# Kernel optimization log

Hardware: AMD Instinct MI355X
Metric: run time of the kernel (lower is better)

The kernel has to match this reference:

```python
import jax, jax.numpy as jnp
import numpy as np

DIMS = 256
HID = 512


def setup_inputs() -> dict:
    key = jax.random.key(0)
    ks = jax.random.split(key, 12)
    s = 0.1
    inp = {
        'x': jax.random.normal(ks[0], (64, 2048, DIMS), dtype=jnp.float32),
        'h': jnp.zeros((64, HID), jnp.float32),
        'c': jnp.zeros((64, HID), jnp.float32),
        'W_j': jax.random.normal(ks[1], (DIMS, HID), jnp.float32) * s,
        'W_i': jax.random.normal(ks[2], (DIMS, HID), jnp.float32) * s,
        'W_f': jax.random.normal(ks[3], (DIMS, HID), jnp.float32) * s,
        'W_o': jax.random.normal(ks[4], (DIMS, HID), jnp.float32) * s,
        'U_j': jax.random.normal(ks[5], (HID, HID), jnp.float32) * s,
        'U_i': jax.random.normal(ks[6], (HID, HID), jnp.float32) * s,
        'U_f': jax.random.normal(ks[7], (HID, HID), jnp.float32) * s,
        'U_o': jax.random.normal(ks[8], (HID, HID), jnp.float32) * s,
        'b_j': jnp.zeros((1, HID), jnp.float32),
        'b_i': jnp.zeros((1, HID), jnp.float32),
        'b_f': jnp.zeros((1, HID), jnp.float32),
        'b_o': jnp.zeros((1, HID), jnp.float32),
        'W_y': jax.random.normal(ks[9], (HID, DIMS), jnp.float32) * s,
        'b_y': jnp.zeros((1, DIMS), jnp.float32),
    }
    return inp


def reference(x, h, c, W_j, W_i, W_f, W_o, U_j, U_i, U_f, U_o,
              b_j, b_i, b_f, b_o, W_y, b_y):
    # Precompute input projections for all timesteps: [B,T,H] -> [T,B,H]
    xj = jnp.einsum('btd,dh->tbh', x, W_j) + b_j
    xi = jnp.einsum('btd,dh->tbh', x, W_i) + b_i
    xf = jnp.einsum('btd,dh->tbh', x, W_f) + b_f
    xo = jnp.einsum('btd,dh->tbh', x, W_o) + b_o

    def step(carry, xs):
        h, c = carry
        pj, pi, pf, po = xs
        # NOTE: module defaults -> j,i,o sigmoid; f tanh; cell activation tanh
        j = jax.nn.sigmoid(pj + h @ U_j)
        i = jax.nn.sigmoid(pi + h @ U_i)
        f = jnp.tanh(pf + h @ U_f)
        o = jax.nn.sigmoid(po + h @ U_o)
        c = f * c + i * j
        h = o * jnp.tanh(c)
        return (h, c), h

    (h_last, c_last), hs = jax.lax.scan(step, (h, c), (xj, xi, xf, xo))
    # hs: [T,B,H] -> y_hat: [B,T,dims]
    y_hat = jnp.einsum('tbh,hd->btd', hs, W_y) + b_y
    return y_hat, h_last, c_last
```

## Files before the change

kernel.cpp:

```cpp
#include <hip/hip_runtime.h>


typedef __attribute__((ext_vector_type(8))) short bf16x8;
typedef __attribute__((ext_vector_type(4))) float f32x4;

#define T_STEPS 2048
#define DIMS 256
#define HID 512

#define NPACK_U  1048576
#define NPACK_WX 524288
#define NPACK_WY 131072

#define OFF_UHI   0u
#define OFF_ULO   2097152u
#define OFF_WXHI  4194304u
#define OFF_WXLO  5242880u
#define OFF_WYHI  6291456u
#define OFF_WYLO  6553600u
#define OFF_HBUF  6815744u
#define OFF_FLAGS 7077888u

__device__ __forceinline__ unsigned short f2bf(float f) {
    unsigned u = __float_as_uint(f);
    return (unsigned short)((u + 0x7fffu + ((u >> 16) & 1u)) >> 16);
}
__device__ __forceinline__ float bf2f(unsigned short h) {
    return __uint_as_float((unsigned)h << 16);
}
__device__ __forceinline__ void split2(float f, unsigned short& hi, unsigned short& lo) {
    hi = f2bf(f);
    lo = f2bf(f - bf2f(hi));
}
__device__ __forceinline__ float sigf(float x) { return 1.0f / (1.0f + __expf(-x)); }
__device__ __forceinline__ float tanhfast(float x) { return 2.0f * sigf(2.0f * x) - 1.0f; }

__global__ void lstm_prep(const float* __restrict__ Uj, const float* __restrict__ Ui,
                          const float* __restrict__ Uf, const float* __restrict__ Uo,
                          const float* __restrict__ Wj, const float* __restrict__ Wi,
                          const float* __restrict__ Wf, const float* __restrict__ Wo,
                          const float* __restrict__ Wy,
                          unsigned short* __restrict__ Uph, unsigned short* __restrict__ Upl,
                          unsigned short* __restrict__ Wxh, unsigned short* __restrict__ Wxl,
                          unsigned short* __restrict__ Wyh, unsigned short* __restrict__ Wyl,
                          unsigned* __restrict__ flags) {
    int idx = blockIdx.x * 256 + threadIdx.x;
    if (idx < NPACK_U) {
        int j = idx & 7, l = (idx >> 3) & 63, ks = (idx >> 9) & 15, nt = (idx >> 13) & 7, s = (idx >> 16) & 15;
        int gate = nt >> 1;
        int hu = s * 32 + (nt & 1) * 16 + (l & 15);
        int k = ks * 32 + ((l >> 4) << 3) + j;
        const float* U = (gate == 0) ? Uj : (gate == 1) ? Ui : (gate == 2) ? Uf : Uo;
        unsigned short hi, lo; split2(U[k * HID + hu], hi, lo);
        Uph[idx] = hi; Upl[idx] = lo;
    } else if (idx < NPACK_U + NPACK_WX) {
        int i2 = idx - NPACK_U;
        int j = i2 & 7, l = (i2 >> 3) & 63, ks = (i2 >> 9) & 7, nt = (i2 >> 12) & 7, s = (i2 >> 15) & 15;
        int gate = nt >> 1;
        int hu = s * 32 + (nt & 1) * 16 + (l & 15);
        int k = ks * 32 + ((l >> 4) << 3) + j;
        const float* W = (gate == 0) ? Wj : (gate == 1) ? Wi : (gate == 2) ? Wf : Wo;
        unsigned short hi, lo; split2(W[k * HID + hu], hi, lo);
        Wxh[i2] = hi; Wxl[i2] = lo;
    } else if (idx < NPACK_U + NPACK_WX + NPACK_WY) {
        int i3 = idx - NPACK_U - NPACK_WX;
        int j = i3 & 7, l = (i3 >> 3) & 63, ks = (i3 >> 9) & 15, s = (i3 >> 13) & 15;
        int k = ks * 32 + ((l >> 4) << 3) + j;
        int col = s * 16 + (l & 15);
        unsigned short hi, lo; split2(Wy[k * DIMS + col], hi, lo);
        Wyh[i3] = hi; Wyl[i3] = lo;
    } else if (idx < NPACK_U + NPACK_WX + NPACK_WY + 64) {
        flags[idx - (NPACK_U + NPACK_WX + NPACK_WY)] = 0u;
    }
}

__global__ __launch_bounds__(256, 1) void lstm_scan(
    const float* __restrict__ x, const float* __restrict__ h0, const float* __restrict__ c0,
    const float* __restrict__ bj_g, const float* __restrict__ bi_g,
    const float* __restrict__ bf_g, const float* __restrict__ bo_g,
    const float* __restrict__ by_g,
    const unsigned short* __restrict__ Uph, const unsigned short* __restrict__ Upl,
    const unsigned short* __restrict__ Wxph, const unsigned short* __restrict__ Wxpl,
    const unsigned short* __restrict__ Wyph, const unsigned short* __restrict__ Wypl,
    unsigned* __restrict__ hbuf32, unsigned* __restrict__ flags,
    float* __restrict__ out)
{
    __shared__ unsigned short xsh[16][264];
    __shared__ unsigned short xsl[16][264];
    __shared__ unsigned short hsh[16][520];
    __shared__ unsigned short hsl[16][520];
    __shared__ float pre[8][16][17];
    __shared__ float yp[4][16][17];
    __shared__ float cbuf[16][32];

    const int tid = threadIdx.x;
    const int wv = tid >> 6;
    const int l = tid & 63;
    const int quad = l >> 4;
    const int lm = l & 15;
    const int g = blockIdx.x >> 4;
    const int s = blockIdx.x & 15;

    bf16x8 bUh[2][16], bUl[2][16], bWxh[2][8], bWxl[2][8], bWyh[4], bWyl[4];
    {
        const bf16x8* UH = reinterpret_cast<const bf16x8*>(Uph);
        const bf16x8* UL = reinterpret_cast<const bf16x8*>(Upl);
        const bf16x8* WH = reinterpret_cast<const bf16x8*>(Wxph);
        const bf16x8* WL = reinterpret_cast<const bf16x8*>(Wxpl);
        const bf16x8* YH = reinterpret_cast<const bf16x8*>(Wyph);
        const bf16x8* YL = reinterpret_cast<const bf16x8*>(Wypl);
        #pragma unroll
        for (int i = 0; i < 2; ++i) {
            int nt = 2 * wv + i;
            #pragma unroll
            for (int ks = 0; ks < 16; ++ks) {
                bUh[i][ks] = UH[((s * 8 + nt) * 16 + ks) * 64 + l];
                bUl[i][ks] = UL[((s * 8 + nt) * 16 + ks) * 64 + l];
            }
            #pragma unroll
            for (int ks = 0; ks < 8; ++ks) {
                bWxh[i][ks] = WH[((s * 8 + nt) * 8 + ks) * 64 + l];
                bWxl[i][ks] = WL[((s * 8 + nt) * 8 + ks) * 64 + l];
            }
        }
        #pragma unroll
        for (int q = 0; q < 4; ++q) {
            bWyh[q] = YH[(s * 16 + wv * 4 + q) * 64 + l];
            bWyl[q] = YL[(s * 16 + wv * 4 + q) * 64 + l];
        }
    }

    const int rr = tid >> 4;
    const int uu = (tid & 15) * 2;
    cbuf[rr][uu]     = c0[(size_t)(g * 16 + rr) * HID + s * 32 + uu];
    cbuf[rr][uu + 1] = c0[(size_t)(g * 16 + rr) * HID + s * 32 + uu + 1];
    float bj0 = bj_g[s * 32 + uu], bj1 = bj_g[s * 32 + uu + 1];
    float bi0 = bi_g[s * 32 + uu], bi1 = bi_g[s * 32 + uu + 1];
    float bf0 = bf_g[s * 32 + uu], bf1 = bf_g[s * 32 + uu + 1];
    float bo0 = bo_g[s * 32 + uu], bo1 = bo_g[s * 32 + uu + 1];
    const float by = by_g[s * 16 + (tid & 15)];

    const int rS = tid >> 4;
    const int cS16 = (tid & 15) * 16;
    const int cS32 = (tid & 15) * 32;
    long long budget = 1ll << 24;

    __syncthreads();

    for (int t = 0; t < T_STEPS; ++t) {
        {
            const float4* xv = reinterpret_cast<const float4*>(
                x + (size_t)(g * 16 + rS) * (T_STEPS * DIMS) + (size_t)t * DIMS + cS16);
            uint4* xdh = reinterpret_cast<uint4*>(&xsh[rS][cS16]);
            uint4* xdl = reinterpret_cast<uint4*>(&xsl[rS][cS16]);
            #pragma unroll
            for (int k = 0; k < 2; ++k) {
                float4 fa = xv[2 * k], fb = xv[2 * k + 1];
                unsigned short h0_, l0_, h1_, l1_, h2_, l2_, h3_, l3_;
                unsigned short h4_, l4_, h5_, l5_, h6_, l6_, h7_, l7_;
                split2(fa.x, h0_, l0_); split2(fa.y, h1_, l1_);
                split2(fa.z, h2_, l2_); split2(fa.w, h3_, l3_);
                split2(fb.x, h4_, l4_); split2(fb.y, h5_, l5_);
                split2(fb.z, h6_, l6_); split2(fb.w, h7_, l7_);
                uint4 uh, ul;
                uh.x = (unsigned)h0_ | ((unsigned)h1_ << 16);
                uh.y = (unsigned)h2_ | ((unsigned)h3_ << 16);
                uh.z = (unsigned)h4_ | ((unsigned)h5_ << 16);
                uh.w = (unsigned)h6_ | ((unsigned)h7_ << 16);
                ul.x = (unsigned)l0_ | ((unsigned)l1_ << 16);
                ul.y = (unsigned)l2_ | ((unsigned)l3_ << 16);
                ul.z = (unsigned)l4_ | ((unsigned)l5_ << 16);
                ul.w = (unsigned)l6_ | ((unsigned)l7_ << 16);
                xdh[k] = uh; xdl[k] = ul;
            }
        }
        __syncthreads();
        f32x4 acc0 = {0.f, 0.f, 0.f, 0.f}, acc1 = {0.f, 0.f, 0.f, 0.f};
        #pragma unroll
        for (int ks = 0; ks < 8; ++ks) {
            bf16x8 ah = *reinterpret_cast<const bf16x8*>(&xsh[lm][ks * 32 + quad * 8]);
            bf16x8 al = *reinterpret_cast<const bf16x8*>(&xsl[lm][ks * 32 + quad * 8]);
            acc0 = __builtin_amdgcn_mfma_f32_16x16x32_bf16(ah, bWxh[0][ks], acc0, 0, 0, 0);
            acc0 = __builtin_amdgcn_mfma_f32_16x16x32_bf16(al, bWxh[0][ks], acc0, 0, 0, 0);
            acc0 = __builtin_amdgcn_mfma_f32_16x16x32_bf16(ah, bWxl[0][ks], acc0, 0, 0, 0);
            acc1 = __builtin_amdgcn_mfma_f32_16x16x32_bf16(ah, bWxh[1][ks], acc1, 0, 0, 0);
            acc1 = __builtin_amdgcn_mfma_f32_16x16x32_bf16(al, bWxh[1][ks], acc1, 0, 0, 0);
            acc1 = __builtin_amdgcn_mfma_f32_16x16x32_bf16(ah, bWxl[1][ks], acc1, 0, 0, 0);
        }

        if (t > 0) {
            const unsigned target = (unsigned)t;
            while (budget > 0) {
                unsigned v = (l < 16)
                    ? __hip_atomic_load(&flags[g * 16 + l], __ATOMIC_RELAXED, __HIP_MEMORY_SCOPE_AGENT)
                    : target;
                if (__all((int)(v >= target))) break;
                --budget;
            }
            asm volatile("" ::: "memory");
            const unsigned base = (unsigned)(((t - 1) & 1) * 32768) + (unsigned)(g * 16 + rS) * 256
                                  + (unsigned)(tid & 15) * 16;
            const unsigned long long* sh = reinterpret_cast<const unsigned long long*>(hbuf32 + base);
            const unsigned long long* sl = reinterpret_cast<const unsigned long long*>(hbuf32 + 16384 + base);
            unsigned long long vh[8], vl[8];
            #pragma unroll
            for (int k = 0; k < 8; ++k)
                vh[k] = __hip_atomic_load(&sh[k], __ATOMIC_RELAXED, __HIP_MEMORY_SCOPE_AGENT);
            #pragma unroll
            for (int k = 0; k < 8; ++k)
                vl[k] = __hip_atomic_load(&sl[k], __ATOMIC_RELAXED, __HIP_MEMORY_SCOPE_AGENT);
            unsigned long long* dh = reinterpret_cast<unsigned long long*>(&hsh[rS][cS32]);
            unsigned long long* dl = reinterpret_cast<unsigned long long*>(&hsl[rS][cS32]);
            #pragma unroll
            for (int k = 0; k < 8; ++k) dh[k] = vh[k];
            #pragma unroll
            for (int k = 0; k < 8; ++k) dl[k] = vl[k];
        } else {
            const float4* hv = reinterpret_cast<const float4*>(
                h0 + (size_t)(g * 16 + rS) * HID + cS32);
            unsigned* hdh = reinterpret_cast<unsigned*>(&hsh[rS][cS32]);
            unsigned* hdl = reinterpret_cast<unsigned*>(&hsl[rS][cS32]);
            #pragma unroll
            for (int k = 0; k < 8; ++k) {
                float4 f = hv[k];
                unsigned short a0, b0, a1, b1, a2, b2, a3, b3;
                split2(f.x, a0, b0); split2(f.y, a1, b1);
                split2(f.z, a2, b2); split2(f.w, a3, b3);
                hdh[2 * k]     = (unsigned)a0 | ((unsigned)a1 << 16);
                hdh[2 * k + 1] = (unsigned)a2 | ((unsigned)a3 << 16);
                hdl[2 * k]     = (unsigned)b0 | ((unsigned)b1 << 16);
                hdl[2 * k + 1] = (unsigned)b2 | ((unsigned)b3 << 16);
            }
        }
        __syncthreads();

        #pragma unroll
        for (int ks = 0; ks < 16; ++ks) {
            bf16x8 ah = *reinterpret_cast<const bf16x8*>(&hsh[lm][ks * 32 + quad * 8]);
            bf16x8 al = *reinterpret_cast<const bf16x8*>(&hsl[lm][ks * 32 + quad * 8]);
            acc0 = __builtin_amdgcn_mfma_f32_16x16x32_bf16(ah, bUh[0][ks], acc0, 0, 0, 0);
            acc0 = __builtin_amdgcn_mfma_f32_16x16x32_bf16(al, bUh[0][ks], acc0, 0, 0, 0);
            acc0 = __builtin_amdgcn_mfma_f32_16x16x32_bf16(ah, bUl[0][ks], acc0, 0, 0, 0);
            acc1 = __builtin_amdgcn_mfma_f32_16x16x32_bf16(ah, bUh[1][ks], acc1, 0, 0, 0);
            acc1 = __builtin_amdgcn_mfma_f32_16x16x32_bf16(al, bUh[1][ks], acc1, 0, 0, 0);
            acc1 = __builtin_amdgcn_mfma_f32_16x16x32_bf16(ah, bUl[1][ks], acc1, 0, 0, 0);
        }
        f32x4 yacc = {0.f, 0.f, 0.f, 0.f};
        if (t > 0) {
            #pragma unroll
            for (int q = 0; q < 4; ++q) {
                bf16x8 ah = *reinterpret_cast<const bf16x8*>(&hsh[lm][(wv * 4 + q) * 32 + quad * 8]);
                bf16x8 al = *reinterpret_cast<const bf16x8*>(&hsl[lm][(wv * 4 + q) * 32 + quad * 8]);
                yacc = __builtin_amdgcn_mfma_f32_16x16x32_bf16(ah, bWyh[q], yacc, 0, 0, 0);
                yacc = __builtin_amdgcn_mfma_f32_16x16x32_bf16(al, bWyh[q], yacc, 0, 0, 0);
                yacc = __builtin_amdgcn_mfma_f32_16x16x32_bf16(ah, bWyl[q], yacc, 0, 0, 0);
            }
        }
        #pragma unroll
        for (int r = 0; r < 4; ++r) {
            pre[2 * wv][quad * 4 + r][lm]     = acc0[r];
            pre[2 * wv + 1][quad * 4 + r][lm] = acc1[r];
            yp[wv][quad * 4 + r][lm]          = yacc[r];
        }
        __syncthreads();

        {
            unsigned short hh[2], hl[2];
            #pragma unroll
            for (int d = 0; d < 2; ++d) {
                int u = uu + d;
                int nt = u >> 4, cc = u & 15;
                float pj = pre[nt][rr][cc]     + (d ? bj1 : bj0);
                float pi = pre[2 + nt][rr][cc] + (d ? bi1 : bi0);
                float pf = pre[4 + nt][rr][cc] + (d ? bf1 : bf0);
                float po = pre[6 + nt][rr][cc] + (d ? bo1 : bo0);
                float jj = sigf(pj), ii = sigf(pi), ff = tanhfast(pf), oo = sigf(po);
                float cn = ff * cbuf[rr][u] + ii * jj;
                cbuf[rr][u] = cn;
                float hn = oo * tanhfast(cn);
                split2(hn, hh[d], hl[d]);
            }
            unsigned pkh = (unsigned)hh[0] | ((unsigned)hh[1] << 16);
            unsigned pkl = (unsigned)hl[0] | ((unsigned)hl[1] << 16);
            unsigned wbase = (unsigned)((t & 1) * 32768) + (unsigned)(g * 16 + rr) * 256
                             + (unsigned)s * 16 + (unsigned)(tid & 15);
            __hip_atomic_store(hbuf32 + wbase, pkh, __ATOMIC_RELAXED, __HIP_MEMORY_SCOPE_AGENT);
            __hip_atomic_store(hbuf32 + 16384 + wbase, pkl, __ATOMIC_RELAXED, __HIP_MEMORY_SCOPE_AGENT);
        }
        asm volatile("s_waitcnt vmcnt(0)" ::: "memory");
        __syncthreads();
        if (tid == 0)
            __hip_atomic_store(&flags[g * 16 + s], (unsigned)(t + 1),
                               __ATOMIC_RELAXED, __HIP_MEMORY_SCOPE_AGENT);

        if (t > 0) {
            int row = tid >> 4, col = tid & 15;
            float yv = yp[0][row][col] + yp[1][row][col] + yp[2][row][col] + yp[3][row][col] + by;
            out[(size_t)(g * 16 + row) * (T_STEPS * DIMS) + (size_t)(t - 1) * DIMS + s * 16 + col] = yv;
        }
    }

    {
        const unsigned target = (unsigned)T_STEPS;
        while (budget > 0) {
            unsigned v = (l < 16)
                ? __hip_atomic_load(&flags[g * 16 + l], __ATOMIC_RELAXED, __HIP_MEMORY_SCOPE_AGENT)
                : target;
            if (__all((int)(v >= target))) break;
            --budget;
        }
        asm volatile("" ::: "memory");
        const unsigned base = (unsigned)(((T_STEPS - 1) & 1) * 32768) + (unsigned)(g * 16 + rS) * 256
                              + (unsigned)(tid & 15) * 16;
        const unsigned long long* sh = reinterpret_cast<const unsigned long long*>(hbuf32 + base);
        const unsigned long long* sl = reinterpret_cast<const unsigned long long*>(hbuf32 + 16384 + base);
        unsigned long long vh[8], vl[8];
        #pragma unroll
        for (int k = 0; k < 8; ++k)
            vh[k] = __hip_atomic_load(&sh[k], __ATOMIC_RELAXED, __HIP_MEMORY_SCOPE_AGENT);
        #pragma unroll
        for (int k = 0; k < 8; ++k)
            vl[k] = __hip_atomic_load(&sl[k], __ATOMIC_RELAXED, __HIP_MEMORY_SCOPE_AGENT);
        unsigned long long* dh = reinterpret_cast<unsigned long long*>(&hsh[rS][cS32]);
        unsigned long long* dl = reinterpret_cast<unsigned long long*>(&hsl[rS][cS32]);
        #pragma unroll
        for (int k = 0; k < 8; ++k) dh[k] = vh[k];
        #pragma unroll
        for (int k = 0; k < 8; ++k) dl[k] = vl[k];
        __syncthreads();
        f32x4 yacc = {0.f, 0.f, 0.f, 0.f};
        #pragma unroll
        for (int q = 0; q < 4; ++q) {
            bf16x8 ah = *reinterpret_cast<const bf16x8*>(&hsh[lm][(wv * 4 + q) * 32 + quad * 8]);
            bf16x8 al = *reinterpret_cast<const bf16x8*>(&hsl[lm][(wv * 4 + q) * 32 + quad * 8]);
            yacc = __builtin_amdgcn_mfma_f32_16x16x32_bf16(ah, bWyh[q], yacc, 0, 0, 0);
            yacc = __builtin_amdgcn_mfma_f32_16x16x32_bf16(al, bWyh[q], yacc, 0, 0, 0);
            yacc = __builtin_amdgcn_mfma_f32_16x16x32_bf16(ah, bWyl[q], yacc, 0, 0, 0);
        }
        #pragma unroll
        for (int r = 0; r < 4; ++r) yp[wv][quad * 4 + r][lm] = yacc[r];
        __syncthreads();
        int row = tid >> 4, col = tid & 15;
        float yv = yp[0][row][col] + yp[1][row][col] + yp[2][row][col] + yp[3][row][col] + by;
        out[(size_t)(g * 16 + row) * (T_STEPS * DIMS) + (size_t)(T_STEPS - 1) * DIMS + s * 16 + col] = yv;

        const size_t YO = (size_t)64 * T_STEPS * DIMS;
        const size_t CO = YO + (size_t)64 * HID;
        #pragma unroll
        for (int d = 0; d < 2; ++d) {
            int u = uu + d;
            out[YO + (size_t)(g * 16 + rr) * HID + s * 32 + u] =
                bf2f(hsh[rr][s * 32 + u]) + bf2f(hsl[rr][s * 32 + u]);
            out[CO + (size_t)(g * 16 + rr) * HID + s * 32 + u] = cbuf[rr][u];
        }
    }
}

extern "C" void kernel_launch(void* const* d_in, const int* in_sizes, int n_in,
                              void* d_out, int out_size, void* d_ws, size_t ws_size,
                              hipStream_t stream) {
    const float* x  = (const float*)d_in[0];
    const float* h0 = (const float*)d_in[1];
    const float* c0 = (const float*)d_in[2];
    const float* Wj = (const float*)d_in[3];
    const float* Wi = (const float*)d_in[4];
    const float* Wf = (const float*)d_in[5];
    const float* Wo = (const float*)d_in[6];
    const float* Uj = (const float*)d_in[7];
    const float* Ui = (const float*)d_in[8];
    const float* Uf = (const float*)d_in[9];
    const float* Uo = (const float*)d_in[10];
    const float* bj = (const float*)d_in[11];
    const float* bi = (const float*)d_in[12];
    const float* bf = (const float*)d_in[13];
    const float* bo = (const float*)d_in[14];
    const float* Wy = (const float*)d_in[15];
    const float* by = (const float*)d_in[16];

    char* ws = (char*)d_ws;
    unsigned short* Uph = (unsigned short*)(ws + OFF_UHI);
    unsigned short* Upl = (unsigned short*)(ws + OFF_ULO);
    unsigned short* Wxh = (unsigned short*)(ws + OFF_WXHI);
    unsigned short* Wxl = (unsigned short*)(ws + OFF_WXLO);
    unsigned short* Wyh = (unsigned short*)(ws + OFF_WYHI);
    unsigned short* Wyl = (unsigned short*)(ws + OFF_WYLO);
    unsigned* hbuf32    = (unsigned*)(ws + OFF_HBUF);
    unsigned* flags     = (unsigned*)(ws + OFF_FLAGS);
    float* out          = (float*)d_out;

    int prep_total = NPACK_U + NPACK_WX + NPACK_WY + 64;
    int prep_blocks = (prep_total + 255) / 256;
    hipLaunchKernelGGL(lstm_prep, dim3(prep_blocks), dim3(256), 0, stream,
                       Uj, Ui, Uf, Uo, Wj, Wi, Wf, Wo, Wy,
                       Uph, Upl, Wxh, Wxl, Wyh, Wyl, flags);
    hipLaunchKernelGGL(lstm_scan, dim3(64), dim3(256), 0, stream,
                       x, h0, c0, bj, bi, bf, bo, by,
                       Uph, Upl, Wxh, Wxl, Wyh, Wyl, hbuf32, flags, out);
}
```

Before: 12.03 ms.

## Split MFMA accumulator chains, move output projection off critical path, prefetch flags early

The single serial accumulator chain per tile becomes three independent accumulators (hi*hi, lo*hi, hi*lo), summed at the end, so consecutive MFMAs no longer wait on each other's result. The W_y output projection for the previous step now runs after the h-store and flag release, taking it off the recurrent critical path. The flag load is issued before the input-projection MFMAs so its latency overlaps compute. In exchange the kernel uses more accumulator registers and adds one extra __syncthreads per step, and the changed summation order alters float rounding slightly.

```diff
diff --git a/kernel.cpp b/kernel.cpp
--- a/kernel.cpp
+++ b/kernel.cpp
@@ -175,26 +175,32 @@
             }
         }
         __syncthreads();
-        f32x4 acc0 = {0.f, 0.f, 0.f, 0.f}, acc1 = {0.f, 0.f, 0.f, 0.f};
+
+        const unsigned target = (unsigned)t;
+        unsigned vearly = target;
+        if (t > 0 && l < 16)
+            vearly = __hip_atomic_load(&flags[g * 16 + l], __ATOMIC_RELAXED, __HIP_MEMORY_SCOPE_AGENT);
+
+        f32x4 aP0 = {0.f, 0.f, 0.f, 0.f}, aQ0 = {0.f, 0.f, 0.f, 0.f}, aR0 = {0.f, 0.f, 0.f, 0.f};
+        f32x4 aP1 = {0.f, 0.f, 0.f, 0.f}, aQ1 = {0.f, 0.f, 0.f, 0.f}, aR1 = {0.f, 0.f, 0.f, 0.f};
         #pragma unroll
         for (int ks = 0; ks < 8; ++ks) {
             bf16x8 ah = *reinterpret_cast<const bf16x8*>(&xsh[lm][ks * 32 + quad * 8]);
             bf16x8 al = *reinterpret_cast<const bf16x8*>(&xsl[lm][ks * 32 + quad * 8]);
-            acc0 = __builtin_amdgcn_mfma_f32_16x16x32_bf16(ah, bWxh[0][ks], acc0, 0, 0, 0);
-            acc0 = __builtin_amdgcn_mfma_f32_16x16x32_bf16(al, bWxh[0][ks], acc0, 0, 0, 0);
-            acc0 = __builtin_amdgcn_mfma_f32_16x16x32_bf16(ah, bWxl[0][ks], acc0, 0, 0, 0);
-            acc1 = __builtin_amdgcn_mfma_f32_16x16x32_bf16(ah, bWxh[1][ks], acc1, 0, 0, 0);
-            acc1 = __builtin_amdgcn_mfma_f32_16x16x32_bf16(al, bWxh[1][ks], acc1, 0, 0, 0);
-            acc1 = __builtin_amdgcn_mfma_f32_16x16x32_bf16(ah, bWxl[1][ks], acc1, 0, 0, 0);
+            aP0 = __builtin_amdgcn_mfma_f32_16x16x32_bf16(ah, bWxh[0][ks], aP0, 0, 0, 0);
+            aQ0 = __builtin_amdgcn_mfma_f32_16x16x32_bf16(al, bWxh[0][ks], aQ0, 0, 0, 0);
+            aR0 = __builtin_amdgcn_mfma_f32_16x16x32_bf16(ah, bWxl[0][ks], aR0, 0, 0, 0);
+            aP1 = __builtin_amdgcn_mfma_f32_16x16x32_bf16(ah, bWxh[1][ks], aP1, 0, 0, 0);
+            aQ1 = __builtin_amdgcn_mfma_f32_16x16x32_bf16(al, bWxh[1][ks], aQ1, 0, 0, 0);
+            aR1 = __builtin_amdgcn_mfma_f32_16x16x32_bf16(ah, bWxl[1][ks], aR1, 0, 0, 0);
         }
 
         if (t > 0) {
-            const unsigned target = (unsigned)t;
-            while (budget > 0) {
-                unsigned v = (l < 16)
+            unsigned v = (l < 16) ? vearly : target;
+            while (!__all((int)(v >= target)) && budget > 0) {
+                v = (l < 16)
                     ? __hip_atomic_load(&flags[g * 16 + l], __ATOMIC_RELAXED, __HIP_MEMORY_SCOPE_AGENT)
                     : target;
-                if (__all((int)(v >= target))) break;
                 --budget;
             }
             asm volatile("" ::: "memory");
@@ -238,29 +244,17 @@
         for (int ks = 0; ks < 16; ++ks) {
             bf16x8 ah = *reinterpret_cast<const bf16x8*>(&hsh[lm][ks * 32 + quad * 8]);
             bf16x8 al = *reinterpret_cast<const bf16x8*>(&hsl[lm][ks * 32 + quad * 8]);
-            acc0 = __builtin_amdgcn_mfma_f32_16x16x32_bf16(ah, bUh[0][ks], acc0, 0, 0, 0);
-            acc0 = __builtin_amdgcn_mfma_f32_16x16x32_bf16(al, bUh[0][ks], acc0, 0, 0, 0);
-            acc0 = __builtin_amdgcn_mfma_f32_16x16x32_bf16(ah, bUl[0][ks], acc0, 0, 0, 0);
-            acc1 = __builtin_amdgcn_mfma_f32_16x16x32_bf16(ah, bUh[1][ks], acc1, 0, 0, 0);
-            acc1 = __builtin_amdgcn_mfma_f32_16x16x32_bf16(al, bUh[1][ks], acc1, 0, 0, 0);
-            acc1 = __builtin_amdgcn_mfma_f32_16x16x32_bf16(ah, bUl[1][ks], acc1, 0, 0, 0);
-        }
-        f32x4 yacc = {0.f, 0.f, 0.f, 0.f};
-        if (t > 0) {
-            #pragma unroll
-            for (int q = 0; q < 4; ++q) {
-                bf16x8 ah = *reinterpret_cast<const bf16x8*>(&hsh[lm][(wv * 4 + q) * 32 + quad * 8]);
-                bf16x8 al = *reinterpret_cast<const bf16x8*>(&hsl[lm][(wv * 4 + q) * 32 + quad * 8]);
-                yacc = __builtin_amdgcn_mfma_f32_16x16x32_bf16(ah, bWyh[q], yacc, 0, 0, 0);
-                yacc = __builtin_amdgcn_mfma_f32_16x16x32_bf16(al, bWyh[q], yacc, 0, 0, 0);
-                yacc = __builtin_amdgcn_mfma_f32_16x16x32_bf16(ah, bWyl[q], yacc, 0, 0, 0);
-            }
+            aP0 = __builtin_amdgcn_mfma_f32_16x16x32_bf16(ah, bUh[0][ks], aP0, 0, 0, 0);
+            aQ0 = __builtin_amdgcn_mfma_f32_16x16x32_bf16(al, bUh[0][ks], aQ0, 0, 0, 0);
+            aR0 = __builtin_amdgcn_mfma_f32_16x16x32_bf16(ah, bUl[0][ks], aR0, 0, 0, 0);
+            aP1 = __builtin_amdgcn_mfma_f32_16x16x32_bf16(ah, bUh[1][ks], aP1, 0, 0, 0);
+            aQ1 = __builtin_amdgcn_mfma_f32_16x16x32_bf16(al, bUh[1][ks], aQ1, 0, 0, 0);
+            aR1 = __builtin_amdgcn_mfma_f32_16x16x32_bf16(ah, bUl[1][ks], aR1, 0, 0, 0);
         }
         #pragma unroll
         for (int r = 0; r < 4; ++r) {
-            pre[2 * wv][quad * 4 + r][lm]     = acc0[r];
-            pre[2 * wv + 1][quad * 4 + r][lm] = acc1[r];
-            yp[wv][quad * 4 + r][lm]          = yacc[r];
+            pre[2 * wv][quad * 4 + r][lm]     = aP0[r] + (aQ0[r] + aR0[r]);
+            pre[2 * wv + 1][quad * 4 + r][lm] = aP1[r] + (aQ1[r] + aR1[r]);
         }
         __syncthreads();
 
@@ -294,6 +288,19 @@
                                __ATOMIC_RELAXED, __HIP_MEMORY_SCOPE_AGENT);
 
         if (t > 0) {
+            f32x4 yP = {0.f, 0.f, 0.f, 0.f}, yQ = {0.f, 0.f, 0.f, 0.f}, yR = {0.f, 0.f, 0.f, 0.f};
+            #pragma unroll
+            for (int q = 0; q < 4; ++q) {
+                bf16x8 ah = *reinterpret_cast<const bf16x8*>(&hsh[lm][(wv * 4 + q) * 32 + quad * 8]);
+                bf16x8 al = *reinterpret_cast<const bf16x8*>(&hsl[lm][(wv * 4 + q) * 32 + quad * 8]);
+                yP = __builtin_amdgcn_mfma_f32_16x16x32_bf16(ah, bWyh[q], yP, 0, 0, 0);
+                yQ = __builtin_amdgcn_mfma_f32_16x16x32_bf16(al, bWyh[q], yQ, 0, 0, 0);
+                yR = __builtin_amdgcn_mfma_f32_16x16x32_bf16(ah, bWyl[q], yR, 0, 0, 0);
+            }
+            #pragma unroll
+            for (int r = 0; r < 4; ++r)
+                yp[wv][quad * 4 + r][lm] = yP[r] + (yQ[r] + yR[r]);
+            __syncthreads();
             int row = tid >> 4, col = tid & 15;
             float yv = yp[0][row][col] + yp[1][row][col] + yp[2][row][col] + yp[3][row][col] + by;
             out[(size_t)(g * 16 + row) * (T_STEPS * DIMS) + (size_t)(t - 1) * DIMS + s * 16 + col] = yv;
@@ -328,17 +335,17 @@
         #pragma unroll
         for (int k = 0; k < 8; ++k) dl[k] = vl[k];
         __syncthreads();
-        f32x4 yacc = {0.f, 0.f, 0.f, 0.f};
+        f32x4 yP = {0.f, 0.f, 0.f, 0.f}, yQ = {0.f, 0.f, 0.f, 0.f}, yR = {0.f, 0.f, 0.f, 0.f};
         #pragma unroll
         for (int q = 0; q < 4; ++q) {
             bf16x8 ah = *reinterpret_cast<const bf16x8*>(&hsh[lm][(wv * 4 + q) * 32 + quad * 8]);
             bf16x8 al = *reinterpret_cast<const bf16x8*>(&hsl[lm][(wv * 4 + q) * 32 + quad * 8]);
-            yacc = __builtin_amdgcn_mfma_f32_16x16x32_bf16(ah, bWyh[q], yacc, 0, 0, 0);
-            yacc = __builtin_amdgcn_mfma_f32_16x16x32_bf16(al, bWyh[q], yacc, 0, 0, 0);
-            yacc = __builtin_amdgcn_mfma_f32_16x16x32_bf16(ah, bWyl[q], yacc, 0, 0, 0);
-        }
-        #pragma unroll
-        for (int r = 0; r < 4; ++r) yp[wv][quad * 4 + r][lm] = yacc[r];
+            yP = __builtin_amdgcn_mfma_f32_16x16x32_bf16(ah, bWyh[q], yP, 0, 0, 0);
+            yQ = __builtin_amdgcn_mfma_f32_16x16x32_bf16(al, bWyh[q], yQ, 0, 0, 0);
+            yR = __builtin_amdgcn_mfma_f32_16x16x32_bf16(ah, bWyl[q], yR, 0, 0, 0);
+        }
+        #pragma unroll
+        for (int r = 0; r < 4; ++r) yp[wv][quad * 4 + r][lm] = yP[r] + (yQ[r] + yR[r]);
         __syncthreads();
         int row = tid >> 4, col = tid & 15;
         float yv = yp[0][row][col] + yp[1][row][col] + yp[2][row][col] + yp[3][row][col] + by;
```

Result: slower. 13.65 ms (+13.4%).

## Precompute input projections in a parallel kernel before the recurrent scan

Applied to the files above, without the earlier changes.

Moves the x·W input projection out of the serial per-timestep loop into a separate fully parallel kernel (2048 blocks) that writes a 1 GiB fp32 buffer of gate pre-activations. The recurrent scan then only loads four float2 values per step and does the h·U matmul. This shortens the serial critical path per step but adds a large write and read of the projection buffer through HBM. A fallback path keeps the original fused scan when the workspace is too small.

```diff
diff --git a/kernel.cpp b/kernel.cpp
--- a/kernel.cpp
+++ b/kernel.cpp
@@ -7,6 +7,7 @@
 #define T_STEPS 2048
 #define DIMS 256
 #define HID 512
+#define TCHUNK 64
 
 #define NPACK_U  1048576
 #define NPACK_WX 524288
@@ -20,6 +21,8 @@
 #define OFF_WYLO  6553600u
 #define OFF_HBUF  6815744u
 #define OFF_FLAGS 7077888u
+#define OFF_PX    8388608ull
+#define PX_BYTES  1073741824ull
 
 __device__ __forceinline__ unsigned short f2bf(float f) {
     unsigned u = __float_as_uint(f);
@@ -74,80 +77,42 @@
     }
 }
 
-__global__ __launch_bounds__(256, 1) void lstm_scan(
-    const float* __restrict__ x, const float* __restrict__ h0, const float* __restrict__ c0,
-    const float* __restrict__ bj_g, const float* __restrict__ bi_g,
-    const float* __restrict__ bf_g, const float* __restrict__ bo_g,
-    const float* __restrict__ by_g,
-    const unsigned short* __restrict__ Uph, const unsigned short* __restrict__ Upl,
+__global__ __launch_bounds__(256, 1) void lstm_prep2(
+    const float* __restrict__ x,
     const unsigned short* __restrict__ Wxph, const unsigned short* __restrict__ Wxpl,
-    const unsigned short* __restrict__ Wyph, const unsigned short* __restrict__ Wypl,
-    unsigned* __restrict__ hbuf32, unsigned* __restrict__ flags,
-    float* __restrict__ out)
+    float* __restrict__ px)
 {
     __shared__ unsigned short xsh[16][264];
     __shared__ unsigned short xsl[16][264];
-    __shared__ unsigned short hsh[16][520];
-    __shared__ unsigned short hsl[16][520];
-    __shared__ float pre[8][16][17];
-    __shared__ float yp[4][16][17];
-    __shared__ float cbuf[16][32];
-
     const int tid = threadIdx.x;
     const int wv = tid >> 6;
     const int l = tid & 63;
     const int quad = l >> 4;
     const int lm = l & 15;
-    const int g = blockIdx.x >> 4;
-    const int s = blockIdx.x & 15;
-
-    bf16x8 bUh[2][16], bUl[2][16], bWxh[2][8], bWxl[2][8], bWyh[4], bWyl[4];
+    const int tc = blockIdx.x & 31;
+    const int gs = blockIdx.x >> 5;
+    const int s = gs & 15;
+    const int g = gs >> 4;
+
+    bf16x8 bWxh[2][8], bWxl[2][8];
     {
-        const bf16x8* UH = reinterpret_cast<const bf16x8*>(Uph);
-        const bf16x8* UL = reinterpret_cast<const bf16x8*>(Upl);
         const bf16x8* WH = reinterpret_cast<const bf16x8*>(Wxph);
         const bf16x8* WL = reinterpret_cast<const bf16x8*>(Wxpl);
-        const bf16x8* YH = reinterpret_cast<const bf16x8*>(Wyph);
-        const bf16x8* YL = reinterpret_cast<const bf16x8*>(Wypl);
         #pragma unroll
         for (int i = 0; i < 2; ++i) {
             int nt = 2 * wv + i;
-            #pragma unroll
-            for (int ks = 0; ks < 16; ++ks) {
-                bUh[i][ks] = UH[((s * 8 + nt) * 16 + ks) * 64 + l];
-                bUl[i][ks] = UL[((s * 8 + nt) * 16 + ks) * 64 + l];
-            }
             #pragma unroll
             for (int ks = 0; ks < 8; ++ks) {
                 bWxh[i][ks] = WH[((s * 8 + nt) * 8 + ks) * 64 + l];
                 bWxl[i][ks] = WL[((s * 8 + nt) * 8 + ks) * 64 + l];
             }
         }
-        #pragma unroll
-        for (int q = 0; q < 4; ++q) {
-            bWyh[q] = YH[(s * 16 + wv * 4 + q) * 64 + l];
-            bWyl[q] = YL[(s * 16 + wv * 4 + q) * 64 + l];
-        }
-    }
-
-    const int rr = tid >> 4;
-    const int uu = (tid & 15) * 2;
-    cbuf[rr][uu]     = c0[(size_t)(g * 16 + rr) * HID + s * 32 + uu];
-    cbuf[rr][uu + 1] = c0[(size_t)(g * 16 + rr) * HID + s * 32 + uu + 1];
-    float bj0 = bj_g[s * 32 + uu], bj1 = bj_g[s * 32 + uu + 1];
-    float bi0 = bi_g[s * 32 + uu], bi1 = bi_g[s * 32 + uu + 1];
-    float bf0 = bf_g[s * 32 + uu], bf1 = bf_g[s * 32 + uu + 1];
-    float bo0 = bo_g[s * 32 + uu], bo1 = bo_g[s * 32 + uu + 1];
-    const float by = by_g[s * 16 + (tid & 15)];
-
+    }
     const int rS = tid >> 4;
     const int cS16 = (tid & 15) * 16;
-    const int cS32 = (tid & 15) * 32;
-    long long budget = 1ll << 24;
-
-    __syncthreads();
-
-    for (int t = 0; t < T_STEPS; ++t) {
+
+    for (int tt = 0; tt < TCHUNK; ++tt) {
+        const int t = tc * TCHUNK + tt;
         {
             const float4* xv = reinterpret_cast<const float4*>(
                 x + (size_t)(g * 16 + rS) * (T_STEPS * DIMS) + (size_t)t * DIMS + cS16);
@@ -187,6 +152,101 @@
             acc1 = __builtin_amdgcn_mfma_f32_16x16x32_bf16(al, bWxh[1][ks], acc1, 0, 0, 0);
             acc1 = __builtin_amdgcn_mfma_f32_16x16x32_bf16(ah, bWxl[1][ks], acc1, 0, 0, 0);
         }
+        {
+            int nt = 2 * wv, gate = nt >> 1, half = nt & 1;
+            #pragma unroll
+            for (int r = 0; r < 4; ++r) {
+                int row = quad * 4 + r;
+                px[((size_t)(g * 16 + row) * T_STEPS + (size_t)t) * 2048
+                   + gate * 512 + s * 32 + half * 16 + lm] = acc0[r];
+            }
+        }
+        {
+            int nt = 2 * wv + 1, gate = nt >> 1, half = nt & 1;
+            #pragma unroll
+            for (int r = 0; r < 4; ++r) {
+                int row = quad * 4 + r;
+                px[((size_t)(g * 16 + row) * T_STEPS + (size_t)t) * 2048
+                   + gate * 512 + s * 32 + half * 16 + lm] = acc1[r];
+            }
+        }
+        __syncthreads();
+    }
+}
+
+__global__ __launch_bounds__(256, 1) void lstm_scan_px(
+    const float* __restrict__ h0, const float* __restrict__ c0,
+    const float* __restrict__ bj_g, const float* __restrict__ bi_g,
+    const float* __restrict__ bf_g, const float* __restrict__ bo_g,
+    const float* __restrict__ by_g,
+    const unsigned short* __restrict__ Uph, const unsigned short* __restrict__ Upl,
+    const unsigned short* __restrict__ Wyph, const unsigned short* __restrict__ Wypl,
+    const float* __restrict__ px,
+    unsigned* __restrict__ hbuf32, unsigned* __restrict__ flags,
+    float* __restrict__ out)
+{
+    __shared__ unsigned short hsh[16][520];
+    __shared__ unsigned short hsl[16][520];
+    __shared__ float pre[8][16][17];
+    __shared__ float yp[4][16][17];
+    __shared__ float cbuf[16][32];
+
+    const int tid = threadIdx.x;
+    const int wv = tid >> 6;
+    const int l = tid & 63;
+    const int quad = l >> 4;
+    const int lm = l & 15;
+    const int g = blockIdx.x >> 4;
+    const int s = blockIdx.x & 15;
+
+    bf16x8 bUh[2][16], bUl[2][16], bWyh[4], bWyl[4];
+    {
+        const bf16x8* UH = reinterpret_cast<const bf16x8*>(Uph);
+        const bf16x8* UL = reinterpret_cast<const bf16x8*>(Upl);
+        const bf16x8* YH = reinterpret_cast<const bf16x8*>(Wyph);
+        const bf16x8* YL = reinterpret_cast<const bf16x8*>(Wypl);
+        #pragma unroll
+        for (int i = 0; i < 2; ++i) {
+            int nt = 2 * wv + i;
+            #pragma unroll
+            for (int ks = 0; ks < 16; ++ks) {
+                bUh[i][ks] = UH[((s * 8 + nt) * 16 + ks) * 64 + l];
+                bUl[i][ks] = UL[((s * 8 + nt) * 16 + ks) * 64 + l];
+            }
+        }
+        #pragma unroll
+        for (int q = 0; q < 4; ++q) {
+            bWyh[q] = YH[(s * 16 + wv * 4 + q) * 64 + l];
+            bWyl[q] = YL[(s * 16 + wv * 4 + q) * 64 + l];
+        }
+    }
+
+    const int rr = tid >> 4;
+    const int uu = (tid & 15) * 2;
+    cbuf[rr][uu]     = c0[(size_t)(g * 16 + rr) * HID + s * 32 + uu];
+    cbuf[rr][uu + 1] = c0[(size_t)(g * 16 + rr) * HID + s * 32 + uu + 1];
+    float bj0 = bj_g[s * 32 + uu], bj1 = bj_g[s * 32 + uu + 1];
+    float bi0 = bi_g[s * 32 + uu], bi1 = bi_g[s * 32 + uu + 1];
+    float bf0 = bf_g[s * 32 + uu], bf1 = bf_g[s * 32 + uu + 1];
+    float bo0 = bo_g[s * 32 + uu], bo1 = bo_g[s * 32 + uu + 1];
+    const float by = by_g[s * 16 + (tid & 15)];
+
+    const int rS = tid >> 4;
+    const int cS32 = (tid & 15) * 32;
+    const float* pxbase = px + (size_t)(g * 16 + rr) * T_STEPS * 2048 + s * 32 + uu;
+    long long budget = 1ll << 24;
+
+    __syncthreads();
+
+    for (int t = 0; t < T_STEPS; ++t) {
+        float2 pxj, pxi, pxf, pxo;
+        {
+            const float* pb = pxbase + (size_t)t * 2048;
+            pxj = *reinterpret_cast<const float2*>(pb);
+            pxi = *reinterpret_cast<const float2*>(pb + 512);
+            pxf = *reinterpret_cast<const float2*>(pb + 1024);
+            pxo = *reinterpret_cast<const float2*>(pb + 1536);
+        }
 
         if (t > 0) {
             const unsigned target = (unsigned)t;
@@ -234,6 +294,7 @@
         }
         __syncthreads();
 
+        f32x4 acc0 = {0.f, 0.f, 0.f, 0.f}, acc1 = {0.f, 0.f, 0.f, 0.f};
         #pragma unroll
         for (int ks = 0; ks < 16; ++ks) {
             bf16x8 ah = *reinterpret_cast<const bf16x8*>(&hsh[lm][ks * 32 + quad * 8]);
@@ -264,6 +325,285 @@
         }
         __syncthreads();
 
+        {
+            unsigned short hh[2], hl[2];
+            #pragma unroll
+            for (int d = 0; d < 2; ++d) {
+                int u = uu + d;
+                int nt = u >> 4, cc = u & 15;
+                float pj = pre[nt][rr][cc]     + (d ? pxj.y : pxj.x) + (d ? bj1 : bj0);
+                float pi = pre[2 + nt][rr][cc] + (d ? pxi.y : pxi.x) + (d ? bi1 : bi0);
+                float pf = pre[4 + nt][rr][cc] + (d ? pxf.y : pxf.x) + (d ? bf1 : bf0);
+                float po = pre[6 + nt][rr][cc] + (d ? pxo.y : pxo.x) + (d ? bo1 : bo0);
+                float jj = sigf(pj), ii = sigf(pi), ff = tanhfast(pf), oo = sigf(po);
+                float cn = ff * cbuf[rr][u] + ii * jj;
+                cbuf[rr][u] = cn;
+                float hn = oo * tanhfast(cn);
+                split2(hn, hh[d], hl[d]);
+            }
+            unsigned pkh = (unsigned)hh[0] | ((unsigned)hh[1] << 16);
+            unsigned pkl = (unsigned)hl[0] | ((unsigned)hl[1] << 16);
+            unsigned wbase = (unsigned)((t & 1) * 32768) + (unsigned)(g * 16 + rr) * 256
+                             + (unsigned)s * 16 + (unsigned)(tid & 15);
+            __hip_atomic_store(hbuf32 + wbase, pkh, __ATOMIC_RELAXED, __HIP_MEMORY_SCOPE_AGENT);
+            __hip_atomic_store(hbuf32 + 16384 + wbase, pkl, __ATOMIC_RELAXED, __HIP_MEMORY_SCOPE_AGENT);
+        }
+        asm volatile("s_waitcnt vmcnt(0)" ::: "memory");
+        __syncthreads();
+        if (tid == 0)
+            __hip_atomic_store(&flags[g * 16 + s], (unsigned)(t + 1),
+                               __ATOMIC_RELAXED, __HIP_MEMORY_SCOPE_AGENT);
+
+        if (t > 0) {
+            int row = tid >> 4, col = tid & 15;
+            float yv = yp[0][row][col] + yp[1][row][col] + yp[2][row][col] + yp[3][row][col] + by;
+            out[(size_t)(g * 16 + row) * (T_STEPS * DIMS) + (size_t)(t - 1) * DIMS + s * 16 + col] = yv;
+        }
+    }
+
+    {
+        const unsigned target = (unsigned)T_STEPS;
+        while (budget > 0) {
+            unsigned v = (l < 16)
+                ? __hip_atomic_load(&flags[g * 16 + l], __ATOMIC_RELAXED, __HIP_MEMORY_SCOPE_AGENT)
+                : target;
+            if (__all((int)(v >= target))) break;
+            --budget;
+        }
+        asm volatile("" ::: "memory");
+        const unsigned base = (unsigned)(((T_STEPS - 1) & 1) * 32768) + (unsigned)(g * 16 + rS) * 256
+                              + (unsigned)(tid & 15) * 16;
+        const unsigned long long* sh = reinterpret_cast<const unsigned long long*>(hbuf32 + base);
+        const unsigned long long* sl = reinterpret_cast<const unsigned long long*>(hbuf32 + 16384 + base);
+        unsigned long long vh[8], vl[8];
+        #pragma unroll
+        for (int k = 0; k < 8; ++k)
+            vh[k] = __hip_atomic_load(&sh[k], __ATOMIC_RELAXED, __HIP_MEMORY_SCOPE_AGENT);
+        #pragma unroll
+        for (int k = 0; k < 8; ++k)
+            vl[k] = __hip_atomic_load(&sl[k], __ATOMIC_RELAXED, __HIP_MEMORY_SCOPE_AGENT);
+        unsigned long long* dh = reinterpret_cast<unsigned long long*>(&hsh[rS][cS32]);
+        unsigned long long* dl = reinterpret_cast<unsigned long long*>(&hsl[rS][cS32]);
+        #pragma unroll
+        for (int k = 0; k < 8; ++k) dh[k] = vh[k];
+        #pragma unroll
+        for (int k = 0; k < 8; ++k) dl[k] = vl[k];
+        __syncthreads();
+        f32x4 yacc = {0.f, 0.f, 0.f, 0.f};
+        #pragma unroll
+        for (int q = 0; q < 4; ++q) {
+            bf16x8 ah = *reinterpret_cast<const bf16x8*>(&hsh[lm][(wv * 4 + q) * 32 + quad * 8]);
+            bf16x8 al = *reinterpret_cast<const bf16x8*>(&hsl[lm][(wv * 4 + q) * 32 + quad * 8]);
+            yacc = __builtin_amdgcn_mfma_f32_16x16x32_bf16(ah, bWyh[q], yacc, 0, 0, 0);
+            yacc = __builtin_amdgcn_mfma_f32_16x16x32_bf16(al, bWyh[q], yacc, 0, 0, 0);
+            yacc = __builtin_amdgcn_mfma_f32_16x16x32_bf16(ah, bWyl[q], yacc, 0, 0, 0);
+        }
+        #pragma unroll
+        for (int r = 0; r < 4; ++r) yp[wv][quad * 4 + r][lm] = yacc[r];
+        __syncthreads();
+        int row = tid >> 4, col = tid & 15;
+        float yv = yp[0][row][col] + yp[1][row][col] + yp[2][row][col] + yp[3][row][col] + by;
+        out[(size_t)(g * 16 + row) * (T_STEPS * DIMS) + (size_t)(T_STEPS - 1) * DIMS + s * 16 + col] = yv;
+
+        const size_t YO = (size_t)64 * T_STEPS * DIMS;
+        const size_t CO = YO + (size_t)64 * HID;
+        #pragma unroll
+        for (int d = 0; d < 2; ++d) {
+            int u = uu + d;
+            out[YO + (size_t)(g * 16 + rr) * HID + s * 32 + u] =
+                bf2f(hsh[rr][s * 32 + u]) + bf2f(hsl[rr][s * 32 + u]);
+            out[CO + (size_t)(g * 16 + rr) * HID + s * 32 + u] = cbuf[rr][u];
+        }
+    }
+}
+
+__global__ __launch_bounds__(256, 1) void lstm_scan_fb(
+    const float* __restrict__ x, const float* __restrict__ h0, const float* __restrict__ c0,
+    const float* __restrict__ bj_g, const float* __restrict__ bi_g,
+    const float* __restrict__ bf_g, const float* __restrict__ bo_g,
+    const float* __restrict__ by_g,
+    const unsigned short* __restrict__ Uph, const unsigned short* __restrict__ Upl,
+    const unsigned short* __restrict__ Wxph, const unsigned short* __restrict__ Wxpl,
+    const unsigned short* __restrict__ Wyph, const unsigned short* __restrict__ Wypl,
+    unsigned* __restrict__ hbuf32, unsigned* __restrict__ flags,
+    float* __restrict__ out)
+{
+    __shared__ unsigned short xsh[16][264];
+    __shared__ unsigned short xsl[16][264];
+    __shared__ unsigned short hsh[16][520];
+    __shared__ unsigned short hsl[16][520];
+    __shared__ float pre[8][16][17];
+    __shared__ float yp[4][16][17];
+    __shared__ float cbuf[16][32];
+
+    const int tid = threadIdx.x;
+    const int wv = tid >> 6;
+    const int l = tid & 63;
+    const int quad = l >> 4;
+    const int lm = l & 15;
+    const int g = blockIdx.x >> 4;
+    const int s = blockIdx.x & 15;
+
+    bf16x8 bUh[2][16], bUl[2][16], bWxh[2][8], bWxl[2][8], bWyh[4], bWyl[4];
+    {
+        const bf16x8* UH = reinterpret_cast<const bf16x8*>(Uph);
+        const bf16x8* UL = reinterpret_cast<const bf16x8*>(Upl);
+        const bf16x8* WH = reinterpret_cast<const bf16x8*>(Wxph);
+        const bf16x8* WL = reinterpret_cast<const bf16x8*>(Wxpl);
+        const bf16x8* YH = reinterpret_cast<const bf16x8*>(Wyph);
+        const bf16x8* YL = reinterpret_cast<const bf16x8*>(Wypl);
+        #pragma unroll
+        for (int i = 0; i < 2; ++i) {
+            int nt = 2 * wv + i;
+            #pragma unroll
+            for (int ks = 0; ks < 16; ++ks) {
+                bUh[i][ks] = UH[((s * 8 + nt) * 16 + ks) * 64 + l];
+                bUl[i][ks] = UL[((s * 8 + nt) * 16 + ks) * 64 + l];
+            }
+            #pragma unroll
+            for (int ks = 0; ks < 8; ++ks) {
+                bWxh[i][ks] = WH[((s * 8 + nt) * 8 + ks) * 64 + l];
+                bWxl[i][ks] = WL[((s * 8 + nt) * 8 + ks) * 64 + l];
+            }
+        }
+        #pragma unroll
+        for (int q = 0; q < 4; ++q) {
+            bWyh[q] = YH[(s * 16 + wv * 4 + q) * 64 + l];
+            bWyl[q] = YL[(s * 16 + wv * 4 + q) * 64 + l];
+        }
+    }
+
+    const int rr = tid >> 4;
+    const int uu = (tid & 15) * 2;
+    cbuf[rr][uu]     = c0[(size_t)(g * 16 + rr) * HID + s * 32 + uu];
+    cbuf[rr][uu + 1] = c0[(size_t)(g * 16 + rr) * HID + s * 32 + uu + 1];
+    float bj0 = bj_g[s * 32 + uu], bj1 = bj_g[s * 32 + uu + 1];
+    float bi0 = bi_g[s * 32 + uu], bi1 = bi_g[s * 32 + uu + 1];
+    float bf0 = bf_g[s * 32 + uu], bf1 = bf_g[s * 32 + uu + 1];
+    float bo0 = bo_g[s * 32 + uu], bo1 = bo_g[s * 32 + uu + 1];
+    const float by = by_g[s * 16 + (tid & 15)];
+
+    const int rS = tid >> 4;
+    const int cS16 = (tid & 15) * 16;
+    const int cS32 = (tid & 15) * 32;
+    long long budget = 1ll << 24;
+
+    __syncthreads();
+
+    for (int t = 0; t < T_STEPS; ++t) {
+        {
+            const float4* xv = reinterpret_cast<const float4*>(
+                x + (size_t)(g * 16 + rS) * (T_STEPS * DIMS) + (size_t)t * DIMS + cS16);
+            uint4* xdh = reinterpret_cast<uint4*>(&xsh[rS][cS16]);
+            uint4* xdl = reinterpret_cast<uint4*>(&xsl[rS][cS16]);
+            #pragma unroll
+            for (int k = 0; k < 2; ++k) {
+                float4 fa = xv[2 * k], fb = xv[2 * k + 1];
+                unsigned short h0_, l0_, h1_, l1_, h2_, l2_, h3_, l3_;
+                unsigned short h4_, l4_, h5_, l5_, h6_, l6_, h7_, l7_;
+                split2(fa.x, h0_, l0_); split2(fa.y, h1_, l1_);
+                split2(fa.z, h2_, l2_); split2(fa.w, h3_, l3_);
+                split2(fb.x, h4_, l4_); split2(fb.y, h5_, l5_);
+                split2(fb.z, h6_, l6_); split2(fb.w, h7_, l7_);
+                uint4 uh, ul;
+                uh.x = (unsigned)h0_ | ((unsigned)h1_ << 16);
+                uh.y = (unsigned)h2_ | ((unsigned)h3_ << 16);
+                uh.z = (unsigned)h4_ | ((unsigned)h5_ << 16);
+                uh.w = (unsigned)h6_ | ((unsigned)h7_ << 16);
+                ul.x = (unsigned)l0_ | ((unsigned)l1_ << 16);
+                ul.y = (unsigned)l2_ | ((unsigned)l3_ << 16);
+                ul.z = (unsigned)l4_ | ((unsigned)l5_ << 16);
+                ul.w = (unsigned)l6_ | ((unsigned)l7_ << 16);
+                xdh[k] = uh; xdl[k] = ul;
+            }
+        }
+        __syncthreads();
+        f32x4 acc0 = {0.f, 0.f, 0.f, 0.f}, acc1 = {0.f, 0.f, 0.f, 0.f};
+        #pragma unroll
+        for (int ks = 0; ks < 8; ++ks) {
+            bf16x8 ah = *reinterpret_cast<const bf16x8*>(&xsh[lm][ks * 32 + quad * 8]);
+            bf16x8 al = *reinterpret_cast<const bf16x8*>(&xsl[lm][ks * 32 + quad * 8]);
+            acc0 = __builtin_amdgcn_mfma_f32_16x16x32_bf16(ah, bWxh[0][ks], acc0, 0, 0, 0);
+            acc0 = __builtin_amdgcn_mfma_f32_16x16x32_bf16(al, bWxh[0][ks], acc0, 0, 0, 0);
+            acc0 = __builtin_amdgcn_mfma_f32_16x16x32_bf16(ah, bWxl[0][ks], acc0, 0, 0, 0);
+            acc1 = __builtin_amdgcn_mfma_f32_16x16x32_bf16(ah, bWxh[1][ks], acc1, 0, 0, 0);
+            acc1 = __builtin_amdgcn_mfma_f32_16x16x32_bf16(al, bWxh[1][ks], acc1, 0, 0, 0);
+            acc1 = __builtin_amdgcn_mfma_f32_16x16x32_bf16(ah, bWxl[1][ks], acc1, 0, 0, 0);
+        }
+        if (t > 0) {
+            const unsigned target = (unsigned)t;
+            while (budget > 0) {
+                unsigned v = (l < 16)
+                    ? __hip_atomic_load(&flags[g * 16 + l], __ATOMIC_RELAXED, __HIP_MEMORY_SCOPE_AGENT)
+                    : target;
+                if (__all((int)(v >= target))) break;
+                --budget;
+            }
+            asm volatile("" ::: "memory");
+            const unsigned base = (unsigned)(((t - 1) & 1) * 32768) + (unsigned)(g * 16 + rS) * 256
+                                  + (unsigned)(tid & 15) * 16;
+            const unsigned long long* sh = reinterpret_cast<const unsigned long long*>(hbuf32 + base);
+            const unsigned long long* sl = reinterpret_cast<const unsigned long long*>(hbuf32 + 16384 + base);
+            unsigned long long vh[8], vl[8];
+            #pragma unroll
+            for (int k = 0; k < 8; ++k)
+                vh[k] = __hip_atomic_load(&sh[k], __ATOMIC_RELAXED, __HIP_MEMORY_SCOPE_AGENT);
+            #pragma unroll
+            for (int k = 0; k < 8; ++k)
+                vl[k] = __hip_atomic_load(&sl[k], __ATOMIC_RELAXED, __HIP_MEMORY_SCOPE_AGENT);
+            unsigned long long* dh = reinterpret_cast<unsigned long long*>(&hsh[rS][cS32]);
+            unsigned long long* dl = reinterpret_cast<unsigned long long*>(&hsl[rS][cS32]);
+            #pragma unroll
+            for (int k = 0; k < 8; ++k) dh[k] = vh[k];
+            #pragma unroll
+            for (int k = 0; k < 8; ++k) dl[k] = vl[k];
+        } else {
+            const float4* hv = reinterpret_cast<const float4*>(
+                h0 + (size_t)(g * 16 + rS) * HID + cS32);
+            unsigned* hdh = reinterpret_cast<unsigned*>(&hsh[rS][cS32]);
+            unsigned* hdl = reinterpret_cast<unsigned*>(&hsl[rS][cS32]);
+            #pragma unroll
+            for (int k = 0; k < 8; ++k) {
+                float4 f = hv[k];
+                unsigned short a0, b0, a1, b1, a2, b2, a3, b3;
+                split2(f.x, a0, b0); split2(f.y, a1, b1);
+                split2(f.z, a2, b2); split2(f.w, a3, b3);
+                hdh[2 * k]     = (unsigned)a0 | ((unsigned)a1 << 16);
+                hdh[2 * k + 1] = (unsigned)a2 | ((unsigned)a3 << 16);
+                hdl[2 * k]     = (unsigned)b0 | ((unsigned)b1 << 16);
+                hdl[2 * k + 1] = (unsigned)b2 | ((unsigned)b3 << 16);
+            }
+        }
+        __syncthreads();
+        #pragma unroll
+        for (int ks = 0; ks < 16; ++ks) {
+            bf16x8 ah = *reinterpret_cast<const bf16x8*>(&hsh[lm][ks * 32 + quad * 8]);
+            bf16x8 al = *reinterpret_cast<const bf16x8*>(&hsl[lm][ks * 32 + quad * 8]);
+            acc0 = __builtin_amdgcn_mfma_f32_16x16x32_bf16(ah, bUh[0][ks], acc0, 0, 0, 0);
+            acc0 = __builtin_amdgcn_mfma_f32_16x16x32_bf16(al, bUh[0][ks], acc0, 0, 0, 0);
+            acc0 = __builtin_amdgcn_mfma_f32_16x16x32_bf16(ah, bUl[0][ks], acc0, 0, 0, 0);
+            acc1 = __builtin_amdgcn_mfma_f32_16x16x32_bf16(ah, bUh[1][ks], acc1, 0, 0, 0);
+            acc1 = __builtin_amdgcn_mfma_f32_16x16x32_bf16(al, bUh[1][ks], acc1, 0, 0, 0);
+            acc1 = __builtin_amdgcn_mfma_f32_16x16x32_bf16(ah, bUl[1][ks], acc1, 0, 0, 0);
+        }
+        f32x4 yacc = {0.f, 0.f, 0.f, 0.f};
+        if (t > 0) {
+            #pragma unroll
+            for (int q = 0; q < 4; ++q) {
+                bf16x8 ah = *reinterpret_cast<const bf16x8*>(&hsh[lm][(wv * 4 + q) * 32 + quad * 8]);
+                bf16x8 al = *reinterpret_cast<const bf16x8*>(&hsl[lm][(wv * 4 + q) * 32 + quad * 8]);
+                yacc = __builtin_amdgcn_mfma_f32_16x16x32_bf16(ah, bWyh[q], yacc, 0, 0, 0);
+                yacc = __builtin_amdgcn_mfma_f32_16x16x32_bf16(al, bWyh[q], yacc, 0, 0, 0);
+                yacc = __builtin_amdgcn_mfma_f32_16x16x32_bf16(ah, bWyl[q], yacc, 0, 0, 0);
+            }
+        }
+        #pragma unroll
+        for (int r = 0; r < 4; ++r) {
+            pre[2 * wv][quad * 4 + r][lm]     = acc0[r];
+            pre[2 * wv + 1][quad * 4 + r][lm] = acc1[r];
+            yp[wv][quad * 4 + r][lm]          = yacc[r];
+        }
+        __syncthreads();
         {
             unsigned short hh[2], hl[2];
             #pragma unroll
@@ -292,7 +632,6 @@
         if (tid == 0)
             __hip_atomic_store(&flags[g * 16 + s], (unsigned)(t + 1),
                                __ATOMIC_RELAXED, __HIP_MEMORY_SCOPE_AGENT);
-
         if (t > 0) {
             int row = tid >> 4, col = tid & 15;
             float yv = yp[0][row][col] + yp[1][row][col] + yp[2][row][col] + yp[3][row][col] + by;
@@ -386,6 +725,7 @@
     unsigned short* Wyl = (unsigned short*)(ws + OFF_WYLO);
     unsigned* hbuf32    = (unsigned*)(ws + OFF_HBUF);
     unsigned* flags     = (unsigned*)(ws + OFF_FLAGS);
+    float* px           = (float*)(ws + OFF_PX);
     float* out          = (float*)d_out;
 
     int prep_total = NPACK_U + NPACK_WX + NPACK_WY + 64;
@@ -393,7 +733,16 @@
     hipLaunchKernelGGL(lstm_prep, dim3(prep_blocks), dim3(256), 0, stream,
                        Uj, Ui, Uf, Uo, Wj, Wi, Wf, Wo, Wy,
                        Uph, Upl, Wxh, Wxl, Wyh, Wyl, flags);
-    hipLaunchKernelGGL(lstm_scan, dim3(64), dim3(256), 0, stream,
-                       x, h0, c0, bj, bi, bf, bo, by,
-                       Uph, Upl, Wxh, Wxl, Wyh, Wyl, hbuf32, flags, out);
+
+    if (ws_size >= OFF_PX + PX_BYTES) {
+        hipLaunchKernelGGL(lstm_prep2, dim3(2048), dim3(256), 0, stream,
+                           x, Wxh, Wxl, px);
+        hipLaunchKernelGGL(lstm_scan_px, dim3(64), dim3(256), 0, stream,
+                           h0, c0, bj, bi, bf, bo, by,
+                           Uph, Upl, Wyh, Wyl, px, hbuf32, flags, out);
+    } else {
+        hipLaunchKernelGGL(lstm_scan_fb, dim3(64), dim3(256), 0, stream,
+                           x, h0, c0, bj, bi, bf, bo, by,
+                           Uph, Upl, Wxh, Wxl, Wyh, Wyl, hbuf32, flags, out);
+    }
 }
```

Result: no change. 12.05 ms (+0.1%).
